# Kernel optimization log

Measured on AMD Instinct MI355X. Metric: run time of the kernel, lower is better.

The kernel has to match this reference:

```python
import jax, jax.numpy as jnp
import numpy as np

B, H, S, D = 2, 16, 2048, 128


def setup_inputs() -> dict:
    key = jax.random.key(0)
    ks = jax.random.split(key, 11)
    s = 1.0 / np.sqrt(D)
    return {
        "query": jax.random.normal(ks[0], (B, H, S, D), dtype=jnp.float32),
        "key": jax.random.normal(ks[1], (B, H, S, D), dtype=jnp.float32),
        "value": jax.random.normal(ks[2], (B, H, S, D), dtype=jnp.float32),
        "Wq": jax.random.normal(ks[3], (D, D), dtype=jnp.float32) * s,
        "bq": jnp.zeros((D,), dtype=jnp.float32),
        "Wk": jax.random.normal(ks[4], (D, D), dtype=jnp.float32) * s,
        "bk": jnp.zeros((D,), dtype=jnp.float32),
        "Wv": jax.random.normal(ks[5], (D, D), dtype=jnp.float32) * s,
        "bv": jnp.zeros((D,), dtype=jnp.float32),
        "Wo": jax.random.normal(ks[6], (D, D), dtype=jnp.float32) * s,
        "bo": jnp.zeros((D,), dtype=jnp.float32),
    }


def reference(query, key, value, Wq, bq, Wk, bk, Wv, bv, Wo, bo):
    # Linear projections (torch Linear: x @ W^T + b) on last dim of [B,H,S,D]
    q = jnp.einsum("bhsd,ed->bhse", query, Wq) + bq
    k = jnp.einsum("bhsd,ed->bhse", key, Wk) + bk
    v = jnp.einsum("bhsd,ed->bhse", value, Wv) + bv
    scale = jnp.sqrt(jnp.asarray(D, dtype=q.dtype))
    q = q / scale
    qk = jnp.einsum("bhse,bhte->bhst", q, k)  # [B,H,S,S] scores
    attn = jax.nn.softmax(qk, axis=-1)
    # dropout_p = 0.0 -> identity
    out = jnp.einsum("bhst,bhtd->bhsd", attn, v)
    out = jnp.einsum("bhsd,ed->bhse", out, Wo) + bo
    return out
```

## Files before the change

kernel.cpp:

```cpp
#include <hip/hip_runtime.h>
#include <hip/hip_bf16.h>
#include <type_traits>
#include <math.h>

typedef __bf16 bf16x8 __attribute__((ext_vector_type(8)));
typedef float floatx4 __attribute__((ext_vector_type(4)));
typedef float floatx16 __attribute__((ext_vector_type(16)));

#define S_LEN 2048
#define D_DIM 128
#define NTOK (2 * 16 * 2048)
#define KVB 64
#define NKV (S_LEN / KVB)

template <typename TIN, typename TOUT>
__device__ __forceinline__ void proj_body4(
    const TIN* __restrict__ x, const float* __restrict__ W,
    const float* __restrict__ b, TOUT* __restrict__ y, float out_scale,
    int chunk0, __bf16 (*Wl)[128]) {
  const int tid = threadIdx.x;
  const int wave = tid >> 6, lane = tid & 63;
  const int g = lane >> 4, lr = lane & 15;

  for (int it = 0; it < 16; ++it) {
    int lin = it * 1024 + tid * 4;
    float4 w4 = *reinterpret_cast<const float4*>(W + lin);
    int r = lin >> 7, c = lin & 127;
    Wl[r][c]     = (__bf16)w4.x;
    Wl[r][c + 1] = (__bf16)w4.y;
    Wl[r][c + 2] = (__bf16)w4.z;
    Wl[r][c + 3] = (__bf16)w4.w;
  }
  __syncthreads();

  float be[8];
#pragma unroll
  for (int nt = 0; nt < 8; ++nt) be[nt] = b[nt * 16 + lr];

  for (int ch = 0; ch < 4; ++ch) {
    const int rbase = (chunk0 + ch) * 64;
    const int arow = rbase + wave * 16 + lr;

    floatx4 acc[8];
#pragma unroll
    for (int i = 0; i < 8; ++i) acc[i] = floatx4{0.f, 0.f, 0.f, 0.f};

#pragma unroll
    for (int kc = 0; kc < 4; ++kc) {
      bf16x8 af;
      const TIN* xp = x + (size_t)arow * D_DIM + kc * 32 + g * 8;
      if constexpr (std::is_same<TIN, float>::value) {
        float4 f0 = *reinterpret_cast<const float4*>(xp);
        float4 f1 = *reinterpret_cast<const float4*>(xp + 4);
        af[0] = (__bf16)f0.x; af[1] = (__bf16)f0.y;
        af[2] = (__bf16)f0.z; af[3] = (__bf16)f0.w;
        af[4] = (__bf16)f1.x; af[5] = (__bf16)f1.y;
        af[6] = (__bf16)f1.z; af[7] = (__bf16)f1.w;
      } else {
        af = *reinterpret_cast<const bf16x8*>(xp);
      }
#pragma unroll
      for (int nt = 0; nt < 8; ++nt) {
        bf16x8 wf = *reinterpret_cast<const bf16x8*>(&Wl[nt * 16 + lr][kc * 32 + g * 8]);
        acc[nt] = __builtin_amdgcn_mfma_f32_16x16x32_bf16(af, wf, acc[nt], 0, 0, 0);
      }
    }

#pragma unroll
    for (int nt = 0; nt < 8; ++nt) {
      int e = nt * 16 + lr;
#pragma unroll
      for (int j = 0; j < 4; ++j) {
        int row = rbase + wave * 16 + g * 4 + j;
        float val = (acc[nt][j] + be[nt]) * out_scale;
        y[(size_t)row * D_DIM + e] = (TOUT)val;
      }
    }
  }
}

__global__ __launch_bounds__(256) void qkv_proj_kernel(
    const float* __restrict__ xq, const float* __restrict__ xk,
    const float* __restrict__ xv, const float* __restrict__ Wq,
    const float* __restrict__ Wk, const float* __restrict__ Wv,
    const float* __restrict__ bq, const float* __restrict__ bk,
    const float* __restrict__ bv, __bf16* yq, __bf16* yk, __bf16* yv,
    float qscale) {
  __shared__ alignas(16) __bf16 Wl[128][128];
  const int which = blockIdx.y;
  const float* x = which == 0 ? xq : which == 1 ? xk : xv;
  const float* W = which == 0 ? Wq : which == 1 ? Wk : Wv;
  const float* b = which == 0 ? bq : which == 1 ? bk : bv;
  __bf16* y = which == 0 ? yq : which == 1 ? yk : yv;
  float sc = which == 0 ? qscale : 1.0f;
  proj_body4<float, __bf16>(x, W, b, y, sc, blockIdx.x * 4, Wl);
}

__global__ __launch_bounds__(256) void o_proj_kernel(
    const __bf16* __restrict__ x, const float* __restrict__ W,
    const float* __restrict__ b, float* __restrict__ y) {
  __shared__ alignas(16) __bf16 Wl[128][128];
  proj_body4<__bf16, float>(x, W, b, y, 1.0f, blockIdx.x * 4, Wl);
}

__device__ __forceinline__ unsigned swz(int row, unsigned byteoff) {
  return byteoff ^ (((unsigned)(row ^ (row >> 3)) & 7u) << 4);
}

__device__ __forceinline__ unsigned pack2(float lo, float hi) {
  union { __bf16 h[2]; unsigned u; } r;
  r.h[0] = (__bf16)lo; r.h[1] = (__bf16)hi;
  return r.u;
}

__global__ __launch_bounds__(256, 2) void attn_kernel(
    const __bf16* __restrict__ q, const __bf16* __restrict__ k,
    const __bf16* __restrict__ v, __bf16* __restrict__ o) {
  __shared__ alignas(16) unsigned char smem[65536];

  const int tid = threadIdx.x;
  const int wave = tid >> 6, lane = tid & 63;
  const int ql = lane & 31;
  const int h = lane >> 5;

  const int bh = blockIdx.x;
  const int qbase = blockIdx.y * 128;
  const __bf16* qp = q + (size_t)bh * S_LEN * D_DIM;
  const __bf16* kp = k + (size_t)bh * S_LEN * D_DIM;
  const __bf16* vp = v + (size_t)bh * S_LEN * D_DIM;
  __bf16* op = o + (size_t)bh * S_LEN * D_DIM;

  const int qrow = qbase + wave * 32 + ql;
  bf16x8 qf[8];
#pragma unroll
  for (int kc = 0; kc < 8; ++kc)
    qf[kc] = *reinterpret_cast<const bf16x8*>(
        qp + (size_t)qrow * D_DIM + kc * 16 + h * 8);

  floatx16 ot[4];
#pragma unroll
  for (int d = 0; d < 4; ++d)
#pragma unroll
    for (int r = 0; r < 16; ++r) ot[d][r] = 0.f;
  float m_r = -1e30f, l_r = 0.f;

  const int pr = (tid >> 4) * 2;
  const int ce = (tid & 15) * 8;

  unsigned ka[16];
#pragma unroll
  for (int kvh = 0; kvh < 2; ++kvh)
#pragma unroll
    for (int kc = 0; kc < 8; ++kc) {
      int row = kvh * 32 + ql;
      ka[kvh * 8 + kc] = swz(row, row * 256u + kc * 32u + h * 16u);
    }
  unsigned va[16];
#pragma unroll
  for (int ks = 0; ks < 4; ++ks)
#pragma unroll
    for (int db = 0; db < 4; ++db) {
      int row = db * 32 + ql;
      va[ks * 4 + db] = 32768u + swz(row, row * 128u + ks * 32u + h * 16u);
    }
  unsigned kw[4];
  {
    int rows[4] = {pr, pr + 1, pr + 32, pr + 33};
#pragma unroll
    for (int i = 0; i < 4; ++i)
      kw[i] = swz(rows[i], rows[i] * 256u + ce * 2u);
  }
  unsigned vw[16];
#pragma unroll
  for (int e = 0; e < 8; ++e) {
    int d = ce + e;
    vw[e * 2]     = 32768u + swz(d, d * 128u + pr * 2u);
    vw[e * 2 + 1] = 32768u + swz(d, d * 128u + (pr + 32) * 2u);
  }

  {
    const __bf16* kr = kp + (size_t)pr * D_DIM + ce;
    const __bf16* vr = vp + (size_t)pr * D_DIM + ce;
    bf16x8 kA0 = *reinterpret_cast<const bf16x8*>(kr);
    bf16x8 kA1 = *reinterpret_cast<const bf16x8*>(kr + D_DIM);
    bf16x8 kB0 = *reinterpret_cast<const bf16x8*>(kr + 32 * D_DIM);
    bf16x8 kB1 = *reinterpret_cast<const bf16x8*>(kr + 33 * D_DIM);
    union { bf16x8 v8; unsigned short s[8]; } vA0, vA1, vB0, vB1;
    vA0.v8 = *reinterpret_cast<const bf16x8*>(vr);
    vA1.v8 = *reinterpret_cast<const bf16x8*>(vr + D_DIM);
    vB0.v8 = *reinterpret_cast<const bf16x8*>(vr + 32 * D_DIM);
    vB1.v8 = *reinterpret_cast<const bf16x8*>(vr + 33 * D_DIM);
    *reinterpret_cast<bf16x8*>(smem + kw[0]) = kA0;
    *reinterpret_cast<bf16x8*>(smem + kw[1]) = kA1;
    *reinterpret_cast<bf16x8*>(smem + kw[2]) = kB0;
    *reinterpret_cast<bf16x8*>(smem + kw[3]) = kB1;
#pragma unroll
    for (int e = 0; e < 8; ++e) {
      unsigned w0 = (unsigned)vA0.s[e] | ((unsigned)vA1.s[e] << 16);
      unsigned w1 = (unsigned)vB0.s[e] | ((unsigned)vB1.s[e] << 16);
      *reinterpret_cast<unsigned*>(smem + vw[e * 2]) = w0;
      *reinterpret_cast<unsigned*>(smem + vw[e * 2 + 1]) = w1;
    }
  }

  const __bf16* krp = kp + ((size_t)KVB + pr) * D_DIM + ce;
  const __bf16* vrp = vp + ((size_t)KVB + pr) * D_DIM + ce;

#pragma unroll 2
  for (int t = 0; t < NKV; ++t) {
    const unsigned cb = (unsigned)(t & 1) * 16384u;
    const bool hn = (t + 1 < NKV);

    __syncthreads();

    bf16x8 kA0, kA1, kB0, kB1;
    union { bf16x8 v8; unsigned short s[8]; } vA0, vA1, vB0, vB1;
    if (hn) {
      kA0 = *reinterpret_cast<const bf16x8*>(krp);
      kA1 = *reinterpret_cast<const bf16x8*>(krp + D_DIM);
      kB0 = *reinterpret_cast<const bf16x8*>(krp + 32 * D_DIM);
      kB1 = *reinterpret_cast<const bf16x8*>(krp + 33 * D_DIM);
      vA0.v8 = *reinterpret_cast<const bf16x8*>(vrp);
      vA1.v8 = *reinterpret_cast<const bf16x8*>(vrp + D_DIM);
      vB0.v8 = *reinterpret_cast<const bf16x8*>(vrp + 32 * D_DIM);
      vB1.v8 = *reinterpret_cast<const bf16x8*>(vrp + 33 * D_DIM);
      krp += (size_t)KVB * D_DIM;
      vrp += (size_t)KVB * D_DIM;
    }

    floatx16 st[2];
#pragma unroll
    for (int kvh = 0; kvh < 2; ++kvh)
#pragma unroll
      for (int r = 0; r < 16; ++r) st[kvh][r] = 0.f;
    __builtin_amdgcn_s_setprio(1);
#pragma unroll
    for (int kc = 0; kc < 8; ++kc) {
      bf16x8 kf0 = *reinterpret_cast<const bf16x8*>(smem + cb + ka[kc]);
      bf16x8 kf1 = *reinterpret_cast<const bf16x8*>(smem + cb + ka[8 + kc]);
      st[0] = __builtin_amdgcn_mfma_f32_32x32x16_bf16(kf0, qf[kc], st[0], 0, 0, 0);
      st[1] = __builtin_amdgcn_mfma_f32_32x32x16_bf16(kf1, qf[kc], st[1], 0, 0, 0);
    }
    __builtin_amdgcn_s_setprio(0);

    float t8[8];
#pragma unroll
    for (int i = 0; i < 8; ++i)
      t8[i] = fmaxf(fmaxf(st[0][i], st[0][i + 8]), fmaxf(st[1][i], st[1][i + 8]));
    float pmax = fmaxf(fmaxf(fmaxf(t8[0], t8[4]), fmaxf(t8[1], t8[5])),
                       fmaxf(fmaxf(t8[2], t8[6]), fmaxf(t8[3], t8[7])));
    pmax = fmaxf(pmax, __shfl_xor(pmax, 32));
    if (!__all(pmax - m_r <= 8.0f)) {
      float mnew = fmaxf(m_r, pmax);
      float sc_f = __builtin_amdgcn_exp2f(m_r - mnew);
      m_r = mnew;
      l_r *= sc_f;
#pragma unroll
      for (int d = 0; d < 4; ++d)
#pragma unroll
        for (int r = 0; r < 16; ++r) ot[d][r] *= sc_f;
    }
#pragma unroll
    for (int kvh = 0; kvh < 2; ++kvh)
#pragma unroll
      for (int r = 0; r < 16; ++r)
        st[kvh][r] = __builtin_amdgcn_exp2f(st[kvh][r] - m_r);
    float s8[8];
#pragma unroll
    for (int i = 0; i < 8; ++i)
      s8[i] = (st[0][i] + st[0][i + 8]) + (st[1][i] + st[1][i + 8]);
    float psum = ((s8[0] + s8[4]) + (s8[1] + s8[5])) +
                 ((s8[2] + s8[6]) + (s8[3] + s8[7]));
    psum += __shfl_xor(psum, 32);
    l_r += psum;

#pragma unroll
    for (int ks = 0; ks < 4; ++ks) {
      const int kvh = ks >> 1;
      const int r2a = (2 * ks) & 3;
      const int r2b = r2a + 1;
      unsigned a0 = pack2(st[kvh][r2a * 4 + 0], st[kvh][r2a * 4 + 1]);
      unsigned a1 = pack2(st[kvh][r2a * 4 + 2], st[kvh][r2a * 4 + 3]);
      unsigned b0 = pack2(st[kvh][r2b * 4 + 0], st[kvh][r2b * 4 + 1]);
      unsigned b1 = pack2(st[kvh][r2b * 4 + 2], st[kvh][r2b * 4 + 3]);
      union { unsigned u[4]; bf16x8 v8; } pw;
#if __has_builtin(__builtin_amdgcn_permlane32_swap)
      {
        auto r0 = __builtin_amdgcn_permlane32_swap(a0, b0, false, false);
        auto r1 = __builtin_amdgcn_permlane32_swap(a1, b1, false, false);
        pw.u[0] = r0[0];
        pw.u[1] = r1[0];
        pw.u[2] = r0[1];
        pw.u[3] = r1[1];
      }
#else
      {
        unsigned a0x = __shfl_xor(a0, 32), a1x = __shfl_xor(a1, 32);
        unsigned b0x = __shfl_xor(b0, 32), b1x = __shfl_xor(b1, 32);
        pw.u[0] = h ? b0x : a0;
        pw.u[1] = h ? b1x : a1;
        pw.u[2] = h ? b0 : a0x;
        pw.u[3] = h ? b1 : a1x;
      }
#endif
      __builtin_amdgcn_s_setprio(1);
#pragma unroll
      for (int db = 0; db < 4; ++db) {
        bf16x8 vf = *reinterpret_cast<const bf16x8*>(smem + cb + va[ks * 4 + db]);
        ot[db] = __builtin_amdgcn_mfma_f32_32x32x16_bf16(vf, pw.v8, ot[db], 0, 0, 0);
      }
      __builtin_amdgcn_s_setprio(0);
    }

    if (hn) {
      const unsigned nb = cb ^ 16384u;
      *reinterpret_cast<bf16x8*>(smem + nb + kw[0]) = kA0;
      *reinterpret_cast<bf16x8*>(smem + nb + kw[1]) = kA1;
      *reinterpret_cast<bf16x8*>(smem + nb + kw[2]) = kB0;
      *reinterpret_cast<bf16x8*>(smem + nb + kw[3]) = kB1;
#pragma unroll
      for (int e = 0; e < 8; ++e) {
        unsigned w0 = (unsigned)vA0.s[e] | ((unsigned)vA1.s[e] << 16);
        unsigned w1 = (unsigned)vB0.s[e] | ((unsigned)vB1.s[e] << 16);
        *reinterpret_cast<unsigned*>(smem + nb + vw[e * 2]) = w0;
        *reinterpret_cast<unsigned*>(smem + nb + vw[e * 2 + 1]) = w1;
      }
    }
  }

  __syncthreads();
  const float inv_l = 1.0f / l_r;
  const int qloc = wave * 32 + ql;
#pragma unroll
  for (int db = 0; db < 4; ++db)
#pragma unroll
    for (int r = 0; r < 16; ++r) {
      int d = db * 32 + (r & 3) + 8 * (r >> 2) + 4 * h;
      *reinterpret_cast<__bf16*>(smem + swz(qloc, qloc * 256u + d * 2u)) =
          (__bf16)(ot[db][r] * inv_l);
    }
  __syncthreads();
#pragma unroll
  for (int it = 0; it < 8; ++it) {
    int r = tid >> 1;
    int c = (tid & 1) * 64 + it * 8;
    bf16x8 val = *reinterpret_cast<const bf16x8*>(smem + swz(r, r * 256u + c * 2u));
    *reinterpret_cast<bf16x8*>(op + (size_t)(qbase + r) * D_DIM + c) = val;
  }
}

extern "C" void kernel_launch(void* const* d_in, const int* in_sizes, int n_in,
                              void* d_out, int out_size, void* d_ws, size_t ws_size,
                              hipStream_t stream) {
  const float* query = (const float*)d_in[0];
  const float* key_  = (const float*)d_in[1];
  const float* value = (const float*)d_in[2];
  const float* Wq = (const float*)d_in[3];
  const float* bq = (const float*)d_in[4];
  const float* Wk = (const float*)d_in[5];
  const float* bk = (const float*)d_in[6];
  const float* Wv = (const float*)d_in[7];
  const float* bv = (const float*)d_in[8];
  const float* Wo = (const float*)d_in[9];
  const float* bo = (const float*)d_in[10];

  __bf16* vws = (__bf16*)d_ws;
  __bf16* aws = vws + (size_t)NTOK * D_DIM;
  __bf16* qws = (__bf16*)d_out;
  __bf16* kws = qws + (size_t)NTOK * D_DIM;

  const float qscale = 0.1275174490036f;

  qkv_proj_kernel<<<dim3(NTOK / 256, 3), dim3(256), 0, stream>>>(
      query, key_, value, Wq, Wk, Wv, bq, bk, bv, qws, kws, vws, qscale);

  attn_kernel<<<dim3(32, 16), dim3(256), 0, stream>>>(qws, kws, vws, aws);

  o_proj_kernel<<<NTOK / 256, dim3(256), 0, stream>>>(aws, Wo, bo, (float*)d_out);
}
```

Baseline: 133.3 us.

## Software-pipeline QK^T one KV tile ahead of softmax and PV

Restructures the attention loop so the QK^T MFMAs for tile t+1 are issued in the same iteration as the softmax and PV work for tile t. K is prefetched two tiles ahead and V one tile ahead, with staggered LDS double buffers. The aim is to let matrix-core work overlap the exp/max/sum VALU work and hide global-load latency. In exchange it holds an extra pair of score accumulators in registers, which may lower occupancy or cause spills, and it adds a second barrier per iteration.

Result: slower. 152.7 us (+14.5%).

```diff
diff --git a/kernel.cpp b/kernel.cpp
--- a/kernel.cpp
+++ b/kernel.cpp
@@ -178,77 +178,112 @@
     vw[e * 2 + 1] = 32768u + swz(d, d * 128u + (pr + 32) * 2u);
   }
 
+  bf16x8 kS0, kS1, kS2, kS3;
+  union { bf16x8 v8; unsigned short s[8]; } vS0, vS1, vS2, vS3;
+
   {
     const __bf16* kr = kp + (size_t)pr * D_DIM + ce;
-    const __bf16* vr = vp + (size_t)pr * D_DIM + ce;
-    bf16x8 kA0 = *reinterpret_cast<const bf16x8*>(kr);
-    bf16x8 kA1 = *reinterpret_cast<const bf16x8*>(kr + D_DIM);
-    bf16x8 kB0 = *reinterpret_cast<const bf16x8*>(kr + 32 * D_DIM);
-    bf16x8 kB1 = *reinterpret_cast<const bf16x8*>(kr + 33 * D_DIM);
-    union { bf16x8 v8; unsigned short s[8]; } vA0, vA1, vB0, vB1;
-    vA0.v8 = *reinterpret_cast<const bf16x8*>(vr);
-    vA1.v8 = *reinterpret_cast<const bf16x8*>(vr + D_DIM);
-    vB0.v8 = *reinterpret_cast<const bf16x8*>(vr + 32 * D_DIM);
-    vB1.v8 = *reinterpret_cast<const bf16x8*>(vr + 33 * D_DIM);
-    *reinterpret_cast<bf16x8*>(smem + kw[0]) = kA0;
-    *reinterpret_cast<bf16x8*>(smem + kw[1]) = kA1;
-    *reinterpret_cast<bf16x8*>(smem + kw[2]) = kB0;
-    *reinterpret_cast<bf16x8*>(smem + kw[3]) = kB1;
-#pragma unroll
-    for (int e = 0; e < 8; ++e) {
-      unsigned w0 = (unsigned)vA0.s[e] | ((unsigned)vA1.s[e] << 16);
-      unsigned w1 = (unsigned)vB0.s[e] | ((unsigned)vB1.s[e] << 16);
-      *reinterpret_cast<unsigned*>(smem + vw[e * 2]) = w0;
-      *reinterpret_cast<unsigned*>(smem + vw[e * 2 + 1]) = w1;
-    }
-  }
-
-  const __bf16* krp = kp + ((size_t)KVB + pr) * D_DIM + ce;
+    bf16x8 a0 = *reinterpret_cast<const bf16x8*>(kr);
+    bf16x8 a1 = *reinterpret_cast<const bf16x8*>(kr + D_DIM);
+    bf16x8 a2 = *reinterpret_cast<const bf16x8*>(kr + 32 * D_DIM);
+    bf16x8 a3 = *reinterpret_cast<const bf16x8*>(kr + 33 * D_DIM);
+    *reinterpret_cast<bf16x8*>(smem + kw[0]) = a0;
+    *reinterpret_cast<bf16x8*>(smem + kw[1]) = a1;
+    *reinterpret_cast<bf16x8*>(smem + kw[2]) = a2;
+    *reinterpret_cast<bf16x8*>(smem + kw[3]) = a3;
+    const __bf16* k1 = kp + ((size_t)KVB + pr) * D_DIM + ce;
+    kS0 = *reinterpret_cast<const bf16x8*>(k1);
+    kS1 = *reinterpret_cast<const bf16x8*>(k1 + D_DIM);
+    kS2 = *reinterpret_cast<const bf16x8*>(k1 + 32 * D_DIM);
+    kS3 = *reinterpret_cast<const bf16x8*>(k1 + 33 * D_DIM);
+    const __bf16* v0 = vp + (size_t)pr * D_DIM + ce;
+    vS0.v8 = *reinterpret_cast<const bf16x8*>(v0);
+    vS1.v8 = *reinterpret_cast<const bf16x8*>(v0 + D_DIM);
+    vS2.v8 = *reinterpret_cast<const bf16x8*>(v0 + 32 * D_DIM);
+    vS3.v8 = *reinterpret_cast<const bf16x8*>(v0 + 33 * D_DIM);
+  }
+  __syncthreads();
+
+  floatx16 stc0, stc1, stn0, stn1;
+#pragma unroll
+  for (int r = 0; r < 16; ++r) { stc0[r] = 0.f; stc1[r] = 0.f; }
+  __builtin_amdgcn_s_setprio(1);
+#pragma unroll
+  for (int kc = 0; kc < 8; ++kc) {
+    bf16x8 kf0 = *reinterpret_cast<const bf16x8*>(smem + ka[kc]);
+    bf16x8 kf1 = *reinterpret_cast<const bf16x8*>(smem + ka[8 + kc]);
+    stc0 = __builtin_amdgcn_mfma_f32_32x32x16_bf16(kf0, qf[kc], stc0, 0, 0, 0);
+    stc1 = __builtin_amdgcn_mfma_f32_32x32x16_bf16(kf1, qf[kc], stc1, 0, 0, 0);
+  }
+  __builtin_amdgcn_s_setprio(0);
+
+  const __bf16* krp = kp + ((size_t)(2 * KVB) + pr) * D_DIM + ce;
   const __bf16* vrp = vp + ((size_t)KVB + pr) * D_DIM + ce;
 
 #pragma unroll 2
   for (int t = 0; t < NKV; ++t) {
-    const unsigned cb = (unsigned)(t & 1) * 16384u;
-    const bool hn = (t + 1 < NKV);
+    const unsigned pK = (unsigned)((t + 1) & 1) * 16384u;
+    const unsigned pV = (unsigned)(t & 1) * 16384u;
+    const bool hasN = (t + 1 < NKV);
+    const bool hasK2 = (t + 2 < NKV);
 
     __syncthreads();
-
-    bf16x8 kA0, kA1, kB0, kB1;
-    union { bf16x8 v8; unsigned short s[8]; } vA0, vA1, vB0, vB1;
-    if (hn) {
-      kA0 = *reinterpret_cast<const bf16x8*>(krp);
-      kA1 = *reinterpret_cast<const bf16x8*>(krp + D_DIM);
-      kB0 = *reinterpret_cast<const bf16x8*>(krp + 32 * D_DIM);
-      kB1 = *reinterpret_cast<const bf16x8*>(krp + 33 * D_DIM);
-      vA0.v8 = *reinterpret_cast<const bf16x8*>(vrp);
-      vA1.v8 = *reinterpret_cast<const bf16x8*>(vrp + D_DIM);
-      vB0.v8 = *reinterpret_cast<const bf16x8*>(vrp + 32 * D_DIM);
-      vB1.v8 = *reinterpret_cast<const bf16x8*>(vrp + 33 * D_DIM);
+    if (hasN) {
+      *reinterpret_cast<bf16x8*>(smem + pK + kw[0]) = kS0;
+      *reinterpret_cast<bf16x8*>(smem + pK + kw[1]) = kS1;
+      *reinterpret_cast<bf16x8*>(smem + pK + kw[2]) = kS2;
+      *reinterpret_cast<bf16x8*>(smem + pK + kw[3]) = kS3;
+    }
+    {
+#pragma unroll
+      for (int e = 0; e < 8; ++e) {
+        unsigned w0 = (unsigned)vS0.s[e] | ((unsigned)vS1.s[e] << 16);
+        unsigned w1 = (unsigned)vS2.s[e] | ((unsigned)vS3.s[e] << 16);
+        *reinterpret_cast<unsigned*>(smem + pV + vw[e * 2]) = w0;
+        *reinterpret_cast<unsigned*>(smem + pV + vw[e * 2 + 1]) = w1;
+      }
+    }
+    __syncthreads();
+
+    if (hasK2) {
+      kS0 = *reinterpret_cast<const bf16x8*>(krp);
+      kS1 = *reinterpret_cast<const bf16x8*>(krp + D_DIM);
+      kS2 = *reinterpret_cast<const bf16x8*>(krp + 32 * D_DIM);
+      kS3 = *reinterpret_cast<const bf16x8*>(krp + 33 * D_DIM);
       krp += (size_t)KVB * D_DIM;
+    }
+    if (hasN) {
+      vS0.v8 = *reinterpret_cast<const bf16x8*>(vrp);
+      vS1.v8 = *reinterpret_cast<const bf16x8*>(vrp + D_DIM);
+      vS2.v8 = *reinterpret_cast<const bf16x8*>(vrp + 32 * D_DIM);
+      vS3.v8 = *reinterpret_cast<const bf16x8*>(vrp + 33 * D_DIM);
       vrp += (size_t)KVB * D_DIM;
     }
 
-    floatx16 st[2];
-#pragma unroll
-    for (int kvh = 0; kvh < 2; ++kvh)
-#pragma unroll
-      for (int r = 0; r < 16; ++r) st[kvh][r] = 0.f;
-    __builtin_amdgcn_s_setprio(1);
-#pragma unroll
-    for (int kc = 0; kc < 8; ++kc) {
-      bf16x8 kf0 = *reinterpret_cast<const bf16x8*>(smem + cb + ka[kc]);
-      bf16x8 kf1 = *reinterpret_cast<const bf16x8*>(smem + cb + ka[8 + kc]);
-      st[0] = __builtin_amdgcn_mfma_f32_32x32x16_bf16(kf0, qf[kc], st[0], 0, 0, 0);
-      st[1] = __builtin_amdgcn_mfma_f32_32x32x16_bf16(kf1, qf[kc], st[1], 0, 0, 0);
-    }
-    __builtin_amdgcn_s_setprio(0);
-
-    float t8[8];
-#pragma unroll
-    for (int i = 0; i < 8; ++i)
-      t8[i] = fmaxf(fmaxf(st[0][i], st[0][i + 8]), fmaxf(st[1][i], st[1][i + 8]));
-    float pmax = fmaxf(fmaxf(fmaxf(t8[0], t8[4]), fmaxf(t8[1], t8[5])),
-                       fmaxf(fmaxf(t8[2], t8[6]), fmaxf(t8[3], t8[7])));
+    if (hasN) {
+#pragma unroll
+      for (int r = 0; r < 16; ++r) { stn0[r] = 0.f; stn1[r] = 0.f; }
+      __builtin_amdgcn_s_setprio(1);
+#pragma unroll
+      for (int kc = 0; kc < 8; ++kc) {
+        bf16x8 kf0 = *reinterpret_cast<const bf16x8*>(smem + pK + ka[kc]);
+        bf16x8 kf1 = *reinterpret_cast<const bf16x8*>(smem + pK + ka[8 + kc]);
+        stn0 = __builtin_amdgcn_mfma_f32_32x32x16_bf16(kf0, qf[kc], stn0, 0, 0, 0);
+        stn1 = __builtin_amdgcn_mfma_f32_32x32x16_bf16(kf1, qf[kc], stn1, 0, 0, 0);
+      }
+      __builtin_amdgcn_s_setprio(0);
+    }
+
+    float m16[16];
+#pragma unroll
+    for (int i = 0; i < 16; ++i) m16[i] = fmaxf(stc0[i], stc1[i]);
+    float a0 = fmaxf(fmaxf(m16[0], m16[1]), m16[2]);
+    float a1 = fmaxf(fmaxf(m16[3], m16[4]), m16[5]);
+    float a2 = fmaxf(fmaxf(m16[6], m16[7]), m16[8]);
+    float a3 = fmaxf(fmaxf(m16[9], m16[10]), m16[11]);
+    float a4 = fmaxf(fmaxf(m16[12], m16[13]), m16[14]);
+    float pmax = fmaxf(fmaxf(fmaxf(a0, a1), a2),
+                       fmaxf(fmaxf(a3, a4), m16[15]));
     pmax = fmaxf(pmax, __shfl_xor(pmax, 32));
     if (!__all(pmax - m_r <= 8.0f)) {
       float mnew = fmaxf(m_r, pmax);
@@ -261,14 +296,14 @@
         for (int r = 0; r < 16; ++r) ot[d][r] *= sc_f;
     }
 #pragma unroll
-    for (int kvh = 0; kvh < 2; ++kvh)
-#pragma unroll
-      for (int r = 0; r < 16; ++r)
-        st[kvh][r] = __builtin_amdgcn_exp2f(st[kvh][r] - m_r);
+    for (int r = 0; r < 16; ++r) {
+      stc0[r] = __builtin_amdgcn_exp2f(stc0[r] - m_r);
+      stc1[r] = __builtin_amdgcn_exp2f(stc1[r] - m_r);
+    }
     float s8[8];
 #pragma unroll
     for (int i = 0; i < 8; ++i)
-      s8[i] = (st[0][i] + st[0][i + 8]) + (st[1][i] + st[1][i + 8]);
+      s8[i] = (stc0[i] + stc0[i + 8]) + (stc1[i] + stc1[i + 8]);
     float psum = ((s8[0] + s8[4]) + (s8[1] + s8[5])) +
                  ((s8[2] + s8[6]) + (s8[3] + s8[7]));
     psum += __shfl_xor(psum, 32);
@@ -276,18 +311,29 @@
 
 #pragma unroll
     for (int ks = 0; ks < 4; ++ks) {
-      const int kvh = ks >> 1;
       const int r2a = (2 * ks) & 3;
       const int r2b = r2a + 1;
-      unsigned a0 = pack2(st[kvh][r2a * 4 + 0], st[kvh][r2a * 4 + 1]);
-      unsigned a1 = pack2(st[kvh][r2a * 4 + 2], st[kvh][r2a * 4 + 3]);
-      unsigned b0 = pack2(st[kvh][r2b * 4 + 0], st[kvh][r2b * 4 + 1]);
-      unsigned b1 = pack2(st[kvh][r2b * 4 + 2], st[kvh][r2b * 4 + 3]);
+      float p0, p1, p2, p3, p4, p5, p6, p7;
+      if (ks < 2) {
+        p0 = stc0[r2a * 4 + 0]; p1 = stc0[r2a * 4 + 1];
+        p2 = stc0[r2a * 4 + 2]; p3 = stc0[r2a * 4 + 3];
+        p4 = stc0[r2b * 4 + 0]; p5 = stc0[r2b * 4 + 1];
+        p6 = stc0[r2b * 4 + 2]; p7 = stc0[r2b * 4 + 3];
+      } else {
+        p0 = stc1[r2a * 4 + 0]; p1 = stc1[r2a * 4 + 1];
+        p2 = stc1[r2a * 4 + 2]; p3 = stc1[r2a * 4 + 3];
+        p4 = stc1[r2b * 4 + 0]; p5 = stc1[r2b * 4 + 1];
+        p6 = stc1[r2b * 4 + 2]; p7 = stc1[r2b * 4 + 3];
+      }
+      unsigned ua0 = pack2(p0, p1);
+      unsigned ua1 = pack2(p2, p3);
+      unsigned ub0 = pack2(p4, p5);
+      unsigned ub1 = pack2(p6, p7);
       union { unsigned u[4]; bf16x8 v8; } pw;
 #if __has_builtin(__builtin_amdgcn_permlane32_swap)
       {
-        auto r0 = __builtin_amdgcn_permlane32_swap(a0, b0, false, false);
-        auto r1 = __builtin_amdgcn_permlane32_swap(a1, b1, false, false);
+        auto r0 = __builtin_amdgcn_permlane32_swap(ua0, ub0, false, false);
+        auto r1 = __builtin_amdgcn_permlane32_swap(ua1, ub1, false, false);
         pw.u[0] = r0[0];
         pw.u[1] = r1[0];
         pw.u[2] = r0[1];
@@ -295,37 +341,24 @@
       }
 #else
       {
-        unsigned a0x = __shfl_xor(a0, 32), a1x = __shfl_xor(a1, 32);
-        unsigned b0x = __shfl_xor(b0, 32), b1x = __shfl_xor(b1, 32);
-        pw.u[0] = h ? b0x : a0;
-        pw.u[1] = h ? b1x : a1;
-        pw.u[2] = h ? b0 : a0x;
-        pw.u[3] = h ? b1 : a1x;
+        unsigned a0x = __shfl_xor(ua0, 32), a1x = __shfl_xor(ua1, 32);
+        unsigned b0x = __shfl_xor(ub0, 32), b1x = __shfl_xor(ub1, 32);
+        pw.u[0] = h ? b0x : ua0;
+        pw.u[1] = h ? b1x : ua1;
+        pw.u[2] = h ? ub0 : a0x;
+        pw.u[3] = h ? ub1 : a1x;
       }
 #endif
       __builtin_amdgcn_s_setprio(1);
 #pragma unroll
       for (int db = 0; db < 4; ++db) {
-        bf16x8 vf = *reinterpret_cast<const bf16x8*>(smem + cb + va[ks * 4 + db]);
+        bf16x8 vf = *reinterpret_cast<const bf16x8*>(smem + pV + va[ks * 4 + db]);
         ot[db] = __builtin_amdgcn_mfma_f32_32x32x16_bf16(vf, pw.v8, ot[db], 0, 0, 0);
       }
       __builtin_amdgcn_s_setprio(0);
     }
 
-    if (hn) {
-      const unsigned nb = cb ^ 16384u;
-      *reinterpret_cast<bf16x8*>(smem + nb + kw[0]) = kA0;
-      *reinterpret_cast<bf16x8*>(smem + nb + kw[1]) = kA1;
-      *reinterpret_cast<bf16x8*>(smem + nb + kw[2]) = kB0;
-      *reinterpret_cast<bf16x8*>(smem + nb + kw[3]) = kB1;
-#pragma unroll
-      for (int e = 0; e < 8; ++e) {
-        unsigned w0 = (unsigned)vA0.s[e] | ((unsigned)vA1.s[e] << 16);
-        unsigned w1 = (unsigned)vB0.s[e] | ((unsigned)vB1.s[e] << 16);
-        *reinterpret_cast<unsigned*>(smem + nb + vw[e * 2]) = w0;
-        *reinterpret_cast<unsigned*>(smem + nb + vw[e * 2 + 1]) = w1;
-      }
-    }
+    if (hasN) { stc0 = stn0; stc1 = stn1; }
   }
 
   __syncthreads();
```
